# Kernel tuning notes

Hardware: AMD Instinct MI355X
Metric: run time of the kernel (lower is better)

## Reference

```python
import jax, jax.numpy as jnp
import numpy as np

D_MODEL = 1024
N_HEADS = 16
N_KV = 8
GROUP = N_HEADS // N_KV  # 2
D_HEAD = D_MODEL // N_HEADS  # 64
SCALE = D_HEAD ** -0.5


def setup_inputs() -> dict:
    key = jax.random.key(0)
    ks = jax.random.split(key, 5)
    s = 0.02
    return {
        "x": jax.random.normal(ks[0], (2, 2048, D_MODEL), dtype=jnp.float32),
        "Wq": jax.random.normal(ks[1], (D_MODEL, D_MODEL), dtype=jnp.float32) * s,
        "Wk": jax.random.normal(ks[2], (N_KV * D_HEAD, D_MODEL), dtype=jnp.float32) * s,
        "Wv": jax.random.normal(ks[3], (N_KV * D_HEAD, D_MODEL), dtype=jnp.float32) * s,
        "Wproj": jax.random.normal(ks[4], (D_MODEL, D_MODEL), dtype=jnp.float32) * s,
    }


def reference(x, Wq, Wk, Wv, Wproj):
    b, t, c = x.shape
    # projections (torch Linear: x @ W.T)
    q = (x @ Wq.T).reshape(b, t, N_KV, GROUP, D_HEAD)  # heads ordered (kv, group)
    k = (x @ Wk.T).reshape(b, t, N_KV, D_HEAD)
    v = (x @ Wv.T).reshape(b, t, N_KV, D_HEAD)
    # repeat_interleave(K/V, group, dim=heads) == broadcast over the group axis,
    # since q head index h maps to kv head h // GROUP.
    scores = jnp.einsum('btkgd,bskd->bkgts', q, k) * SCALE  # (b, kv, g, t, s)
    attn = jax.nn.softmax(scores, axis=-1)
    y = jnp.einsum('bkgts,bskd->btkgd', attn, v)  # (b, t, kv, g, d)
    y = y.reshape(b, t, c)
    return y @ Wproj.T
```

## Files before the change

kernel.cpp:

```cpp
#include <hip/hip_runtime.h>


#define SEQ    2048
#define CDIM   1024
#define KVDIM  512
#define SCL2E  0.18033688011112042f

typedef __attribute__((ext_vector_type(8))) short   bf16x8;
typedef __attribute__((ext_vector_type(4))) float   f32x4;
typedef unsigned short ushort_t;

__device__ __forceinline__ ushort_t f2bf(float f) {
    unsigned u = __float_as_uint(f);
    u += 0x7FFFu + ((u >> 16) & 1u);
    return (ushort_t)(u >> 16);
}
__device__ __forceinline__ float bf2f(ushort_t h) {
    return __uint_as_float(((unsigned)h) << 16);
}
__device__ __forceinline__ void load_lds16(const void* g, void* l) {
    __builtin_amdgcn_global_load_lds(
        (const __attribute__((address_space(1))) void*)g,
        (__attribute__((address_space(3))) void*)l, 16, 0, 0);
}

__global__ __launch_bounds__(256) void cvt_bf16(
    const float* __restrict__ x,  const float* __restrict__ wq,
    const float* __restrict__ wk, const float* __restrict__ wv,
    const float* __restrict__ wp,
    ushort_t* __restrict__ xh,  ushort_t* __restrict__ wqh,
    ushort_t* __restrict__ wkh, ushort_t* __restrict__ wvh,
    ushort_t* __restrict__ wph)
{
    const int i = blockIdx.x * 256 + threadIdx.x;
    const float* src; ushort_t* dst; int off;
    if (i < 1048576)      { src = x;  dst = xh;  off = i; }
    else if (i < 1310720) { src = wq; dst = wqh; off = i - 1048576; }
    else if (i < 1441792) { src = wk; dst = wkh; off = i - 1310720; }
    else if (i < 1572864) { src = wv; dst = wvh; off = i - 1441792; }
    else                  { src = wp; dst = wph; off = i - 1572864; }
    const float4 v = ((const float4*)src)[off];
    ushort4 h;
    h.x = f2bf(v.x); h.y = f2bf(v.y); h.z = f2bf(v.z); h.w = f2bf(v.w);
    ((ushort4*)dst)[off] = h;
}

__global__ __launch_bounds__(256, 4) void gemm64(
    const ushort_t* __restrict__ A, int K,
    const ushort_t* __restrict__ B1, void* __restrict__ C1, int N1, int epi1, float sc1,
    const ushort_t* __restrict__ B2, void* __restrict__ C2, int N2, int epi2, float sc2,
    const ushort_t* __restrict__ B3, void* __restrict__ C3, int N3, int epi3, float sc3)
{
    __shared__ ushort_t sA[128 * 64];
    __shared__ ushort_t sB[64 * 64];

    const int tid = threadIdx.x, wv = tid >> 6, lane = tid & 63;
    const int lm = lane & 15, quad = lane >> 4;
    const int m0 = blockIdx.y * 128;

    const int t1 = N1 >> 6, t2 = N2 >> 6;
    const int bx = blockIdx.x;
    const ushort_t* B; void* Cv; int n0, Nout, epi; float sc;
    if (bx < t1)           { B = B1; Cv = C1; Nout = N1; epi = epi1; sc = sc1; n0 = bx * 64; }
    else if (bx < t1 + t2) { B = B2; Cv = C2; Nout = N2; epi = epi2; sc = sc2; n0 = (bx - t1) * 64; }
    else                   { B = B3; Cv = C3; Nout = N3; epi = epi3; sc = sc3; n0 = (bx - t1 - t2) * 64; }

    const int mh = wv >> 1, nh = wv & 1;
    const int srow = lane >> 3;
    const int scol = ((lane & 7) ^ ((lane >> 3) & 7)) * 8;

    f32x4 acc[4][2] = {};

    for (int k0 = 0; k0 < K; k0 += 64) {
        __syncthreads();
        #pragma unroll
        for (int i = 0; i < 6; ++i) {
            const int g = wv * 6 + i;
            if (g < 16)
                load_lds16(A + (size_t)(m0 + g * 8 + srow) * K + k0 + scol, sA + g * 512);
            else
                load_lds16(B + (size_t)(n0 + (g - 16) * 8 + srow) * K + k0 + scol, sB + (g - 16) * 512);
        }
        __syncthreads();

        #pragma unroll
        for (int ks = 0; ks < 2; ++ks) {
            const int co = ((ks * 4 + quad) ^ (lm & 7)) * 8;
            bf16x8 a[4], b[2];
            #pragma unroll
            for (int mt = 0; mt < 4; ++mt)
                a[mt] = *(const bf16x8*)&sA[(mh * 64 + mt * 16 + lm) * 64 + co];
            #pragma unroll
            for (int nt = 0; nt < 2; ++nt)
                b[nt] = *(const bf16x8*)&sB[(nh * 32 + nt * 16 + lm) * 64 + co];
            #pragma unroll
            for (int mt = 0; mt < 4; ++mt)
                #pragma unroll
                for (int nt = 0; nt < 2; ++nt)
                    acc[mt][nt] = __builtin_amdgcn_mfma_f32_16x16x32_bf16(a[mt], b[nt], acc[mt][nt], 0, 0, 0);
        }
    }

    if (epi == 0) {
        float* C = (float*)Cv;
        #pragma unroll
        for (int mt = 0; mt < 4; ++mt)
            #pragma unroll
            for (int nt = 0; nt < 2; ++nt)
                #pragma unroll
                for (int r = 0; r < 4; ++r)
                    C[(size_t)(m0 + mh * 64 + mt * 16 + quad * 4 + r) * Nout + n0 + nh * 32 + nt * 16 + lm]
                        = acc[mt][nt][r];
    } else {
        ushort_t* C = (ushort_t*)Cv;
        #pragma unroll
        for (int mt = 0; mt < 4; ++mt)
            #pragma unroll
            for (int nt = 0; nt < 2; ++nt)
                #pragma unroll
                for (int r = 0; r < 4; ++r)
                    C[(size_t)(m0 + mh * 64 + mt * 16 + quad * 4 + r) * Nout + n0 + nh * 32 + nt * 16 + lm]
                        = f2bf(acc[mt][nt][r] * sc);
    }
}

__global__ __launch_bounds__(256) void vtrans_kernel(
    const float* __restrict__ v, ushort_t* __restrict__ vt)
{
    __shared__ float tile[64][65];
    const int t0  = blockIdx.x * 64;
    const int bkv = blockIdx.y;
    const int r   = threadIdx.x >> 2;
    const int c0  = (threadIdx.x & 3) * 16;

    const float* src = v + (size_t)((bkv >> 3) * SEQ + t0 + r) * KVDIM + (bkv & 7) * 64 + c0;
    #pragma unroll
    for (int i = 0; i < 4; ++i) {
        const float4 f = *(const float4*)(src + i * 4);
        tile[r][c0 + i*4 + 0] = f.x;
        tile[r][c0 + i*4 + 1] = f.y;
        tile[r][c0 + i*4 + 2] = f.z;
        tile[r][c0 + i*4 + 3] = f.w;
    }
    __syncthreads();
    ushort_t* dst = vt + (size_t)(bkv * 64 + r) * SEQ + t0 + c0;
    #pragma unroll
    for (int i = 0; i < 4; ++i) {
        ushort4 u;
        u.x = f2bf(tile[c0 + i*4 + 0][r]);
        u.y = f2bf(tile[c0 + i*4 + 1][r]);
        u.z = f2bf(tile[c0 + i*4 + 2][r]);
        u.w = f2bf(tile[c0 + i*4 + 3][r]);
        *(ushort4*)(dst + i * 4) = u;
    }
}

__global__ __launch_bounds__(256, 2) void attn4(
    const ushort_t* __restrict__ Qh, const ushort_t* __restrict__ Kh,
    const ushort_t* __restrict__ Vth, ushort_t* __restrict__ Yh)
{
    __shared__ ushort_t sK[2][64 * 64];
    __shared__ ushort_t sV[2][64 * 64];

    const int tid = threadIdx.x, wv = tid >> 6, lane = tid & 63;
    const int lm = lane & 15, quad = lane >> 4;
    const int b = blockIdx.y >> 4, h = blockIdx.y & 15, kvh = h >> 1;
    const int t0 = blockIdx.x * 128, tq0 = t0 + wv * 32;

    bf16x8 qh[2][2];
    #pragma unroll
    for (int qg = 0; qg < 2; ++qg) {
        const size_t rb = (size_t)(b * SEQ + tq0 + qg * 16 + lm) * CDIM + h * 64;
        #pragma unroll
        for (int ks = 0; ks < 2; ++ks)
            qh[qg][ks] = *(const bf16x8*)(Qh + rb + ks * 32 + quad * 8);
    }

    const ushort_t* gK = Kh  + (size_t)b * SEQ * KVDIM + kvh * 64;
    const ushort_t* gV = Vth + (size_t)(b * 8 + kvh) * 64 * SEQ;

    const int sit  = (wv & 1) * 4;
    const int srow = lane >> 3;
    const int scol = ((lane & 7) ^ ((lane >> 3) & 7)) * 8;

    int krow[4];
    #pragma unroll
    for (int it = 0; it < 4; ++it) {
        const int lr = (sit + it) * 8 + srow;
        krow[it] = (lr & 0x20) | ((lr & 0x10) >> 2) | ((lr & 0x0C) << 1) | (lr & 3);
    }

    float l_r[2] = {0.0f, 0.0f};
    f32x4 O[2][4] = {};

    if (wv < 2) {
        #pragma unroll
        for (int it = 0; it < 4; ++it)
            load_lds16(gK + (size_t)krow[it] * KVDIM + scol,
                       &sK[0][(sit + it) * 512]);
    } else {
        #pragma unroll
        for (int it = 0; it < 4; ++it)
            load_lds16(gV + (size_t)((sit + it) * 8 + srow) * SEQ + scol,
                       &sV[0][(sit + it) * 512]);
    }

    typedef union { bf16x8 v; unsigned u[4]; } pku;

    for (int kt = 0; kt < SEQ / 64; ++kt) {
        const int cur = kt & 1;
        __syncthreads();

        if (kt + 1 < SEQ / 64) {
            const int s1 = (kt + 1) * 64;
            if (wv < 2) {
                #pragma unroll
                for (int it = 0; it < 4; ++it)
                    load_lds16(gK + (size_t)(s1 + krow[it]) * KVDIM + scol,
                               &sK[cur ^ 1][(sit + it) * 512]);
            } else {
                #pragma unroll
                for (int it = 0; it < 4; ++it)
                    load_lds16(gV + (size_t)((sit + it) * 8 + srow) * SEQ + s1 + scol,
                               &sV[cur ^ 1][(sit + it) * 512]);
            }
        }

        f32x4 st[2][4] = {};
        #pragma unroll
        for (int sti = 0; sti < 4; ++sti)
            #pragma unroll
            for (int ks = 0; ks < 2; ++ks) {
                const int off = (sti * 16 + lm) * 64 + (((ks * 4 + quad) ^ (lm & 7)) * 8);
                const bf16x8 kf = *(const bf16x8*)&sK[cur][off];
                #pragma unroll
                for (int qg = 0; qg < 2; ++qg)
                    st[qg][sti] = __builtin_amdgcn_mfma_f32_16x16x32_bf16(kf, qh[qg][ks], st[qg][sti], 0, 0, 0);
            }

        pku pa[2][2];
        #pragma unroll
        for (int qg = 0; qg < 2; ++qg)
            #pragma unroll
            for (int sti = 0; sti < 4; ++sti) {
                const float p0 = __builtin_amdgcn_exp2f(st[qg][sti][0]);
                const float p1 = __builtin_amdgcn_exp2f(st[qg][sti][1]);
                const float p2 = __builtin_amdgcn_exp2f(st[qg][sti][2]);
                const float p3 = __builtin_amdgcn_exp2f(st[qg][sti][3]);
                l_r[qg] += (p0 + p1) + (p2 + p3);
                pa[qg][sti >> 1].u[(sti & 1) * 2 + 0] =
                    __builtin_amdgcn_perm(__float_as_uint(p1), __float_as_uint(p0), 0x07060302u);
                pa[qg][sti >> 1].u[(sti & 1) * 2 + 1] =
                    __builtin_amdgcn_perm(__float_as_uint(p3), __float_as_uint(p2), 0x07060302u);
            }

        #pragma unroll
        for (int ks = 0; ks < 2; ++ks) {
            const int co = ((ks * 4 + quad) ^ (lm & 7)) * 8;
            #pragma unroll
            for (int dt = 0; dt < 4; ++dt) {
                const bf16x8 vt = *(const bf16x8*)&sV[cur][(dt * 16 + lm) * 64 + co];
                #pragma unroll
                for (int qg = 0; qg < 2; ++qg)
                    O[qg][dt] = __builtin_amdgcn_mfma_f32_16x16x32_bf16(pa[qg][ks].v, vt, O[qg][dt], 0, 0, 0);
            }
        }
    }

    #pragma unroll
    for (int qg = 0; qg < 2; ++qg) {
        l_r[qg] += __shfl_xor(l_r[qg], 16);
        l_r[qg] += __shfl_xor(l_r[qg], 32);
    }
    #pragma unroll
    for (int qg = 0; qg < 2; ++qg)
        #pragma unroll
        for (int r = 0; r < 4; ++r) {
            const float lq = __shfl(l_r[qg], (lane & 48) | (quad * 4 + r));
            const float inv = 1.0f / lq;
            const int t = tq0 + qg * 16 + quad * 4 + r;
            const size_t rowb = (size_t)(b * SEQ + t) * CDIM + h * 64;
            #pragma unroll
            for (int dt = 0; dt < 4; ++dt)
                Yh[rowb + dt * 16 + lm] = f2bf(O[qg][dt][r] * inv);
        }
}

extern "C" void kernel_launch(void* const* d_in, const int* in_sizes, int n_in,
                              void* d_out, int out_size, void* d_ws, size_t ws_size,
                              hipStream_t stream)
{
    const float* x     = (const float*)d_in[0];
    const float* Wq    = (const float*)d_in[1];
    const float* Wk    = (const float*)d_in[2];
    const float* Wv    = (const float*)d_in[3];
    const float* Wproj = (const float*)d_in[4];
    float* out = (float*)d_out;

    const int M = 2 * SEQ;

    char* p = (char*)d_ws;
    ushort_t* xh   = (ushort_t*)p; p += (size_t)M * CDIM * 2;
    ushort_t* wqh  = (ushort_t*)p; p += (size_t)CDIM * CDIM * 2;
    ushort_t* wkh  = (ushort_t*)p; p += (size_t)KVDIM * CDIM * 2;
    ushort_t* wvh  = (ushort_t*)p; p += (size_t)KVDIM * CDIM * 2;
    ushort_t* wph  = (ushort_t*)p; p += (size_t)CDIM * CDIM * 2;
    ushort_t* qh   = (ushort_t*)p; p += (size_t)M * CDIM * 2;
    ushort_t* kh   = (ushort_t*)p; p += (size_t)M * KVDIM * 2;
    float*    vbuf = (float*)p;    p += (size_t)M * KVDIM * 4;
    ushort_t* vth  = (ushort_t*)p; p += (size_t)M * KVDIM * 2;
    ushort_t* yh = xh;

    dim3 blk(256);

    cvt_bf16<<<dim3(7168), blk, 0, stream>>>(
        x, Wq, Wk, Wv, Wproj, xh, wqh, wkh, wvh, wph);

    gemm64<<<dim3(32, 32), blk, 0, stream>>>(
        xh, CDIM,
        wqh, qh,   CDIM,  3, SCL2E,
        wkh, kh,   KVDIM, 3, 1.0f,
        wvh, vbuf, KVDIM, 0, 1.0f);

    vtrans_kernel<<<dim3(SEQ / 64, 16), blk, 0, stream>>>(vbuf, vth);

    attn4<<<dim3(SEQ / 128, 32), blk, 0, stream>>>(qh, kh, vth, yh);

    gemm64<<<dim3(16, 32), blk, 0, stream>>>(
        yh, CDIM,
        wph, out, CDIM, 0, 1.0f,
        nullptr, nullptr, 0, 0, 1.0f,
        nullptr, nullptr, 0, 0, 1.0f);
}
```

Baseline: 169.0 us.

## Double KV tile to 128 keys per iteration with setprio around MFMA phases

The attention kernel now processes 128 keys per loop iteration instead of 64, which halves the number of barriers and loop iterations and doubles the LDS buffers for K and V. The V tile gets a new 128-wide row layout with XOR swizzling. The row-sum accumulation is split into two accumulators, and s_setprio raises wave priority during the MFMA phases. The cost is more LDS and registers per block, which may hurt occupancy at 2 blocks per SIMD, and the new swizzle has to line up with the read indexing.

Result: faster. 163.1 us (-3.5%).

```diff
diff --git a/kernel.cpp b/kernel.cpp
--- a/kernel.cpp
+++ b/kernel.cpp
@@ -159,8 +159,8 @@
     const ushort_t* __restrict__ Qh, const ushort_t* __restrict__ Kh,
     const ushort_t* __restrict__ Vth, ushort_t* __restrict__ Yh)
 {
-    __shared__ ushort_t sK[2][64 * 64];
-    __shared__ ushort_t sV[2][64 * 64];
+    __shared__ ushort_t sK[2][128 * 64];
+    __shared__ ushort_t sV[2][64 * 128];
 
     const int tid = threadIdx.x, wv = tid >> 6, lane = tid & 63;
     const int lm = lane & 15, quad = lane >> 4;
@@ -179,56 +179,65 @@
     const ushort_t* gK = Kh  + (size_t)b * SEQ * KVDIM + kvh * 64;
     const ushort_t* gV = Vth + (size_t)(b * 8 + kvh) * 64 * SEQ;
 
-    const int sit  = (wv & 1) * 4;
+    const int g0 = (wv & 1) * 8;
+
     const int srow = lane >> 3;
     const int scol = ((lane & 7) ^ ((lane >> 3) & 7)) * 8;
 
-    int krow[4];
-    #pragma unroll
-    for (int it = 0; it < 4; ++it) {
-        const int lr = (sit + it) * 8 + srow;
-        krow[it] = (lr & 0x20) | ((lr & 0x10) >> 2) | ((lr & 0x0C) << 1) | (lr & 3);
-    }
-
-    float l_r[2] = {0.0f, 0.0f};
+    int krow[8];
+    #pragma unroll
+    for (int it = 0; it < 8; ++it) {
+        const int lr = (g0 + it) * 8 + srow;
+        krow[it] = (lr & 0x60) | ((lr & 0x10) >> 2) | ((lr & 0x0C) << 1) | (lr & 3);
+    }
+
+    const int vrow = lane >> 4;
+    const int vpos = lane & 15;
+
+    float l_a[2] = {0.0f, 0.0f}, l_b[2] = {0.0f, 0.0f};
     f32x4 O[2][4] = {};
 
     if (wv < 2) {
         #pragma unroll
-        for (int it = 0; it < 4; ++it)
+        for (int it = 0; it < 8; ++it)
             load_lds16(gK + (size_t)krow[it] * KVDIM + scol,
-                       &sK[0][(sit + it) * 512]);
+                       &sK[0][(g0 + it) * 512]);
     } else {
         #pragma unroll
-        for (int it = 0; it < 4; ++it)
-            load_lds16(gV + (size_t)((sit + it) * 8 + srow) * SEQ + scol,
-                       &sV[0][(sit + it) * 512]);
+        for (int it = 0; it < 8; ++it) {
+            const int d = (g0 + it) * 4 + vrow;
+            load_lds16(gV + (size_t)d * SEQ + (vpos ^ (d & 7)) * 8,
+                       &sV[0][(g0 + it) * 512]);
+        }
     }
 
     typedef union { bf16x8 v; unsigned u[4]; } pku;
 
-    for (int kt = 0; kt < SEQ / 64; ++kt) {
+    for (int kt = 0; kt < SEQ / 128; ++kt) {
         const int cur = kt & 1;
         __syncthreads();
 
-        if (kt + 1 < SEQ / 64) {
-            const int s1 = (kt + 1) * 64;
+        if (kt + 1 < SEQ / 128) {
+            const int s1 = (kt + 1) * 128;
             if (wv < 2) {
                 #pragma unroll
-                for (int it = 0; it < 4; ++it)
+                for (int it = 0; it < 8; ++it)
                     load_lds16(gK + (size_t)(s1 + krow[it]) * KVDIM + scol,
-                               &sK[cur ^ 1][(sit + it) * 512]);
+                               &sK[cur ^ 1][(g0 + it) * 512]);
             } else {
                 #pragma unroll
-                for (int it = 0; it < 4; ++it)
-                    load_lds16(gV + (size_t)((sit + it) * 8 + srow) * SEQ + s1 + scol,
-                               &sV[cur ^ 1][(sit + it) * 512]);
+                for (int it = 0; it < 8; ++it) {
+                    const int d = (g0 + it) * 4 + vrow;
+                    load_lds16(gV + (size_t)d * SEQ + s1 + (vpos ^ (d & 7)) * 8,
+                               &sV[cur ^ 1][(g0 + it) * 512]);
+                }
             }
         }
 
-        f32x4 st[2][4] = {};
-        #pragma unroll
-        for (int sti = 0; sti < 4; ++sti)
+        f32x4 st[2][8] = {};
+        __builtin_amdgcn_s_setprio(1);
+        #pragma unroll
+        for (int sti = 0; sti < 8; ++sti)
             #pragma unroll
             for (int ks = 0; ks < 2; ++ks) {
                 const int off = (sti * 16 + lm) * 64 + (((ks * 4 + quad) ^ (lm & 7)) * 8);
@@ -237,38 +246,44 @@
                 for (int qg = 0; qg < 2; ++qg)
                     st[qg][sti] = __builtin_amdgcn_mfma_f32_16x16x32_bf16(kf, qh[qg][ks], st[qg][sti], 0, 0, 0);
             }
-
-        pku pa[2][2];
+        __builtin_amdgcn_s_setprio(0);
+
+        pku pa[2][4];
         #pragma unroll
         for (int qg = 0; qg < 2; ++qg)
             #pragma unroll
-            for (int sti = 0; sti < 4; ++sti) {
+            for (int sti = 0; sti < 8; ++sti) {
                 const float p0 = __builtin_amdgcn_exp2f(st[qg][sti][0]);
                 const float p1 = __builtin_amdgcn_exp2f(st[qg][sti][1]);
                 const float p2 = __builtin_amdgcn_exp2f(st[qg][sti][2]);
                 const float p3 = __builtin_amdgcn_exp2f(st[qg][sti][3]);
-                l_r[qg] += (p0 + p1) + (p2 + p3);
+                if (sti & 1) l_b[qg] += (p0 + p1) + (p2 + p3);
+                else         l_a[qg] += (p0 + p1) + (p2 + p3);
                 pa[qg][sti >> 1].u[(sti & 1) * 2 + 0] =
                     __builtin_amdgcn_perm(__float_as_uint(p1), __float_as_uint(p0), 0x07060302u);
                 pa[qg][sti >> 1].u[(sti & 1) * 2 + 1] =
                     __builtin_amdgcn_perm(__float_as_uint(p3), __float_as_uint(p2), 0x07060302u);
             }
 
-        #pragma unroll
-        for (int ks = 0; ks < 2; ++ks) {
+        __builtin_amdgcn_s_setprio(1);
+        #pragma unroll
+        for (int ks = 0; ks < 4; ++ks) {
             const int co = ((ks * 4 + quad) ^ (lm & 7)) * 8;
             #pragma unroll
             for (int dt = 0; dt < 4; ++dt) {
-                const bf16x8 vt = *(const bf16x8*)&sV[cur][(dt * 16 + lm) * 64 + co];
+                const bf16x8 vt = *(const bf16x8*)&sV[cur][(dt * 16 + lm) * 128 + co];
                 #pragma unroll
                 for (int qg = 0; qg < 2; ++qg)
                     O[qg][dt] = __builtin_amdgcn_mfma_f32_16x16x32_bf16(pa[qg][ks].v, vt, O[qg][dt], 0, 0, 0);
             }
         }
-    }
-
+        __builtin_amdgcn_s_setprio(0);
+    }
+
+    float l_r[2];
     #pragma unroll
     for (int qg = 0; qg < 2; ++qg) {
+        l_r[qg] = l_a[qg] + l_b[qg];
         l_r[qg] += __shfl_xor(l_r[qg], 16);
         l_r[qg] += __shfl_xor(l_r[qg], 32);
     }
```
